# Optimization experiments

Measured on AMD Instinct MI355X. Metric: run time of the kernel, lower is better.

The kernel has to match this reference:

```python
import jax, jax.numpy as jnp
import numpy as np

C = 128  # num_hidden[-1]; nheads = 1 so dim == C
L, H, W = 16, 96, 96


def conv5(x, w):
    # x: [N, Cin, H, W], w: [1, Cin, 5, 5]; padding=2 -> SAME
    return jax.lax.conv_general_dilated(
        x, w, window_strides=(1, 1), padding=[(2, 2), (2, 2)],
        dimension_numbers=('NCHW', 'OIHW', 'NCHW'))


def setup_inputs() -> dict:
    key = jax.random.key(0)
    ks = jax.random.split(key, 9)
    s = 0.05
    return dict(
        x=jax.random.normal(ks[0], (L, C, H, W), jnp.float32),
        Wq=jax.random.normal(ks[1], (C, C), jnp.float32) * s,
        bq=jax.random.normal(ks[2], (C,), jnp.float32) * s,
        Wk=jax.random.normal(ks[3], (C, C), jnp.float32) * s,
        bk=jax.random.normal(ks[4], (C,), jnp.float32) * s,
        Wv=jax.random.normal(ks[5], (C, C), jnp.float32) * s,
        bv=jax.random.normal(ks[6], (C,), jnp.float32) * s,
        Wa=jax.random.normal(ks[7], (1, 2 * C, 5, 5), jnp.float32) * s,
        ba=jax.random.normal(ks[8], (1,), jnp.float32) * s,
    )


def reference(x, Wq, bq, Wk, bk, Wv, bv, Wa, ba):
    # 1x1 convs == per-pixel linear maps
    Q = jnp.einsum('lchw,dc->ldhw', x, Wq) + bq[None, :, None, None]
    K = jnp.einsum('lchw,dc->ldhw', x, Wk) + bk[None, :, None, None]
    V = jnp.einsum('lchw,dc->ldhw', x, Wv) + bv[None, :, None, None]
    # conv5x5(cat(Qi, Kj)) = conv5x5(Qi; Wa_q) + conv5x5(Kj; Wa_k) + ba
    Aq = conv5(Q, Wa[:, :C])[:, 0]   # [L, H, W]
    Ak = conv5(K, Wa[:, C:])[:, 0]   # [L, H, W]
    S = Aq[:, None] + Ak[None, :] + ba[0]       # [L, L, H, W] score maps H_ij
    A = jax.nn.softmax(S, axis=1)               # softmax over key frame j
    out = jnp.einsum('ijhw,jchw->ichw', A, V)   # weighted sum of V over j
    return out
```

## Files before the change

kernel.cpp:

```cpp
#include <hip/hip_runtime.h>


#define HW    9216
#define HDIM  96
#define WDIM  96
#define CDIM  128
#define WP    28

__device__ __forceinline__ void fma4(float4& a, const float4& x, const float4& s) {
    a.x += x.x * s.x; a.y += x.y * s.y; a.z += x.z * s.z; a.w += x.w * s.w;
}
__device__ __forceinline__ void axpy4(float4& o, float w, const float4& v) {
    o.x += w * v.x; o.y += w * v.y; o.z += w * v.z; o.w += w * v.w;
}

__global__ void k_prep(const float* __restrict__ Wk, const float* __restrict__ Wa,
                       const float* __restrict__ Wv,
                       float* __restrict__ weffp, float* __restrict__ wvt) {
    const int b = blockIdx.x;
    if (b < 14) {
        int idx = b * 256 + threadIdx.x;
        if (idx < 128 * WP) {
            int cp = idx / WP, tap = idx % WP;
            float s = 0.f;
            if (tap < 25)
                for (int c = 0; c < 128; ++c)
                    s += Wk[c * 128 + cp] * Wa[(128 + c) * 25 + tap];
            weffp[idx] = s;
        }
    } else {
        int idx = (b - 14) * 256 + threadIdx.x;
        wvt[(idx & 127) * 128 + (idx >> 7)] = Wv[idx];
    }
}

__global__ __launch_bounds__(256) void k_z(const float* __restrict__ x,
                                           const float* __restrict__ weffp,
                                           float* __restrict__ z) {
    __shared__ float red[4][25][64];
    const int tid  = threadIdx.x;
    const int wav  = __builtin_amdgcn_readfirstlane(tid >> 6);
    const int lane = tid & 63;
    const int j    = blockIdx.y;
    const int px0  = blockIdx.x * 128;

    const float* wg = weffp + wav * 32 * WP;
    const float* xb = x + ((size_t)j * CDIM + wav * 32) * HW + px0 + lane;

    float accA[25], accB[25];
    #pragma unroll
    for (int t = 0; t < 25; ++t) { accA[t] = 0.f; accB[t] = 0.f; }

    #pragma unroll 4
    for (int c = 0; c < 32; ++c) {
        const float* xc = xb + (size_t)c * HW;
        float xa = xc[0];
        float xbv = xc[64];
        #pragma unroll
        for (int t = 0; t < 25; ++t) {
            float wv = wg[c * WP + t];
            accA[t] = fmaf(wv, xa, accA[t]);
            accB[t] = fmaf(wv, xbv, accB[t]);
        }
    }

    float* zb = z + (size_t)j * 25 * HW + px0;

    #pragma unroll
    for (int t = 0; t < 25; ++t) red[wav][t][lane] = accA[t];
    __syncthreads();
    #pragma unroll
    for (int it = 0; it < 7; ++it) {
        int idx = it * 256 + tid;
        if (idx < 1600) {
            int t = idx >> 6, p = idx & 63;
            zb[(size_t)t * HW + p] = (red[0][t][p] + red[1][t][p])
                                   + (red[2][t][p] + red[3][t][p]);
        }
    }
    __syncthreads();

    #pragma unroll
    for (int t = 0; t < 25; ++t) red[wav][t][lane] = accB[t];
    __syncthreads();
    #pragma unroll
    for (int it = 0; it < 7; ++it) {
        int idx = it * 256 + tid;
        if (idx < 1600) {
            int t = idx >> 6, p = idx & 63;
            zb[(size_t)t * HW + 64 + p] = (red[0][t][p] + red[1][t][p])
                                        + (red[2][t][p] + red[3][t][p]);
        }
    }
}

__global__ __launch_bounds__(256) void k_ak(const float* __restrict__ z,
                                            float* __restrict__ ak) {
    const int j  = blockIdx.y;
    const int px = (blockIdx.x * 256 + threadIdx.x) * 4;
    const int h  = px / WDIM, cb = px % WDIM;
    const bool cok0 = (cb > 0);
    const bool cok2 = (cb < WDIM - 4);
    const float4 zf = make_float4(0.f, 0.f, 0.f, 0.f);
    const float* zb = z + (size_t)j * 25 * HW + px;

    float s0 = 0.f, s1 = 0.f, s2 = 0.f, s3 = 0.f;
    #pragma unroll
    for (int kh = 0; kh < 5; ++kh) {
        const bool rok = (unsigned)(h + kh - 2) < (unsigned)HDIM;
        const float* rp = zb + (kh * 5) * HW + (kh - 2) * WDIM;
        #pragma unroll
        for (int kw = 0; kw < 5; ++kw) {
            const float* tp = rp + kw * HW;
            float4 qa = (rok && cok0) ? *(const float4*)(tp - 4) : zf;
            float4 qb = (rok        ) ? *(const float4*)(tp)     : zf;
            float4 qc = (rok && cok2) ? *(const float4*)(tp + 4) : zf;
            float win[12] = {qa.x, qa.y, qa.z, qa.w, qb.x, qb.y, qb.z, qb.w,
                             qc.x, qc.y, qc.z, qc.w};
            s0 += win[kw + 2];
            s1 += win[kw + 3];
            s2 += win[kw + 4];
            s3 += win[kw + 5];
        }
    }
    float4 o = make_float4(s0, s1, s2, s3);
    *(float4*)(ak + (size_t)j * HW + px) = o;
}

__global__ __launch_bounds__(192) void k_conv(const float* __restrict__ x,
                                              const float* __restrict__ weffp,
                                              float* __restrict__ part) {
    const int j  = blockIdx.x;
    const int rt = blockIdx.y;
    const int g  = blockIdx.z;
    const int c0 = g * 16;
    __shared__ float tile[36 * 104];
    __shared__ float wsm[16 * WP];
    const int tid = threadIdx.x;
    for (int i = tid; i < 16 * WP; i += 192) wsm[i] = weffp[c0 * WP + i];
    const int cq = tid % 24;
    const int rg = tid / 24;
    const int r0 = rg * 4;
    const int rowbase = rt * 32;

    float4 acc[4];
    acc[0] = acc[1] = acc[2] = acc[3] = make_float4(0.f, 0.f, 0.f, 0.f);

    for (int ch = 0; ch < 16; ++ch) {
        const float* xc = x + (size_t)(j * CDIM + c0 + ch) * HW;
        __syncthreads();
        for (int idx = tid; idx < 36 * 26; idx += 192) {
            int r = idx / 26, q = idx % 26;
            int gr = rowbase - 2 + r;
            int gc = q * 4 - 4;
            float4 v = make_float4(0.f, 0.f, 0.f, 0.f);
            if (gr >= 0 && gr < HDIM && gc >= 0 && gc < WDIM)
                v = *(const float4*)(xc + gr * WDIM + gc);
            *(float4*)(tile + r * 104 + q * 4) = v;
        }
        __syncthreads();
        const float* wc = wsm + ch * WP;
        for (int rr = 0; rr < 8; ++rr) {
            const float* trow = tile + (r0 + rr) * 104 + cq * 4;
            float4 a  = *(const float4*)(trow);
            float4 b  = *(const float4*)(trow + 4);
            float4 c4 = *(const float4*)(trow + 8);
            float win[12] = {a.x, a.y, a.z, a.w, b.x, b.y, b.z, b.w,
                             c4.x, c4.y, c4.z, c4.w};
            #pragma unroll
            for (int orow = 0; orow < 4; ++orow) {
                int kh = rr - orow;
                if (kh < 0 || kh > 4) continue;
                #pragma unroll
                for (int kw = 0; kw < 5; ++kw) {
                    float w = wc[kh * 5 + kw];
                    acc[orow].x += w * win[kw + 2];
                    acc[orow].y += w * win[kw + 3];
                    acc[orow].z += w * win[kw + 4];
                    acc[orow].w += w * win[kw + 5];
                }
            }
        }
    }
    float* pr = part + (size_t)(g * 16 + j) * HW;
    #pragma unroll
    for (int orow = 0; orow < 4; ++orow) {
        int row = rowbase + r0 + orow;
        *(float4*)(pr + row * WDIM + cq * 4) = acc[orow];
    }
}

__global__ void k_combine(const float* __restrict__ part, float* __restrict__ ak) {
    const int j  = blockIdx.y;
    const int px = blockIdx.x * 256 + threadIdx.x;
    float s = 0.f;
    #pragma unroll
    for (int g = 0; g < 8; ++g) s += part[(size_t)(g * 16 + j) * HW + px];
    ak[(size_t)j * HW + px] = s;
}

__global__ __launch_bounds__(256) void k_xbar(const float* __restrict__ x,
                                              const float* __restrict__ ak,
                                              float* __restrict__ xbar) {
    const int b  = blockIdx.x;
    const int cp = b / 9;
    const int px = (b % 9) * 1024 + threadIdx.x * 4;

    float4 av[16];
    #pragma unroll
    for (int j = 0; j < 16; ++j)
        av[j] = *(const float4*)(ak + (size_t)j * HW + px);

    float4 m = av[0];
    #pragma unroll
    for (int j = 1; j < 16; ++j) {
        m.x = fmaxf(m.x, av[j].x); m.y = fmaxf(m.y, av[j].y);
        m.z = fmaxf(m.z, av[j].z); m.w = fmaxf(m.w, av[j].w);
    }
    float4 tot = make_float4(0.f, 0.f, 0.f, 0.f);
    #pragma unroll
    for (int j = 0; j < 16; ++j) {
        av[j].x = __expf(av[j].x - m.x); av[j].y = __expf(av[j].y - m.y);
        av[j].z = __expf(av[j].z - m.z); av[j].w = __expf(av[j].w - m.w);
        tot.x += av[j].x; tot.y += av[j].y; tot.z += av[j].z; tot.w += av[j].w;
    }
    float4 inv = make_float4(1.f / tot.x, 1.f / tot.y, 1.f / tot.z, 1.f / tot.w);

    float4 acc = make_float4(0.f, 0.f, 0.f, 0.f);
    #pragma unroll
    for (int j = 0; j < 16; ++j) {
        float4 xv = *(const float4*)(x + (size_t)(j * CDIM + cp) * HW + px);
        fma4(acc, xv, av[j]);
    }
    acc.x *= inv.x; acc.y *= inv.y; acc.z *= inv.z; acc.w *= inv.w;
    *(float4*)(xbar + (size_t)cp * HW + px) = acc;
}

__global__ __launch_bounds__(256) void k_mat(const float* __restrict__ xbar,
                                             const float* __restrict__ wvt,
                                             const float* __restrict__ bv,
                                             float* __restrict__ out) {
    __shared__ float lx[128 * 16];
    const int b    = blockIdx.x;
    const int half = blockIdx.y;
    const int tile = (b & 7) * 72 + (b >> 3);
    const int px0  = tile * 16;
    const int tid  = threadIdx.x;

    #pragma unroll
    for (int i = 0; i < 2; ++i) {
        int lin = tid + i * 256;
        int cp = lin >> 2, q = lin & 3;
        *(float4*)(lx + cp * 16 + q * 4) =
            *(const float4*)(xbar + (size_t)cp * HW + px0 + q * 4);
    }
    __syncthreads();

    const int q = tid & 3;
    const int c = half * 64 + (tid >> 2);
    float4 o = make_float4(0.f, 0.f, 0.f, 0.f);
    #pragma unroll 4
    for (int cp = 0; cp < 128; ++cp) {
        float4 xv = *(const float4*)(lx + cp * 16 + q * 4);
        axpy4(o, wvt[cp * 128 + c], xv);
    }
    float bb = bv[c];
    o.x += bb; o.y += bb; o.z += bb; o.w += bb;

    for (int i = 0; i < 16; ++i) {
        float* ob = out + (size_t)(i * CDIM + c) * HW + px0 + q * 4;
        *(float4*)(ob) = o;
    }
}

extern "C" void kernel_launch(void* const* d_in, const int* in_sizes, int n_in,
                              void* d_out, int out_size, void* d_ws, size_t ws_size,
                              hipStream_t stream) {
    const float* x  = (const float*)d_in[0];
    const float* Wk = (const float*)d_in[3];
    const float* Wv = (const float*)d_in[5];
    const float* bv = (const float*)d_in[6];
    const float* Wa = (const float*)d_in[7];
    float* out = (float*)d_out;

    char* ws = (char*)d_ws;
    float* weffp = (float*)(ws);
    float* wvt   = (float*)(ws + 16384);

    k_prep<<<78, 256, 0, stream>>>(Wk, Wa, Wv, weffp, wvt);

    const size_t Z_BYTES  = (size_t)16 * 25 * HW * 4;
    const size_t AK_BYTES = (size_t)16 * HW * 4;
    const size_t NEED_BIG = 81920 + Z_BYTES + AK_BYTES;

    if (ws_size >= NEED_BIG) {
        float* z   = (float*)(ws + 81920);
        float* akb = (float*)(ws + 81920 + Z_BYTES);
        float* xb  = (float*)(ws + 81920);
        k_z   <<<dim3(72, 16),  256, 0, stream>>>(x, weffp, z);
        k_ak  <<<dim3(9, 16),   256, 0, stream>>>(z, akb);
        k_xbar<<<1152,          256, 0, stream>>>(x, akb, xb);
        k_mat <<<dim3(576, 2),  256, 0, stream>>>(xb, wvt, bv, out);
    } else {
        float* part = (float*)(ws + 81920);
        float* akb  = (float*)(ws + 81920 + 4718592);
        float* xb   = (float*)(ws + 81920);
        k_conv   <<<dim3(16, 3, 8), 192, 0, stream>>>(x, weffp, part);
        k_combine<<<dim3(36, 16),   256, 0, stream>>>(part, akb);
        k_xbar   <<<1152,           256, 0, stream>>>(x, akb, xb);
        k_mat    <<<dim3(576, 2),   256, 0, stream>>>(xb, wvt, bv, out);
    }
}
```

Measured before the change: 74.06 us.

## Compute per-tap key projection z with bf16 MFMA instead of FP32 FMAs

Replaces the scalar FP32 k_z kernel, which accumulated 25 tap projections per pixel across four waves and reduced them through shared memory, with k_zm. The new kernel uses 16x16x32 bf16 MFMA instructions, with the effective weights pre-converted to bf16 by a new k_wb kernel and x converted to bf16 on the fly. This removes the LDS reduction and the large scalar FMA count, but lowers the precision of the attention logits and adds an extra small kernel launch. The x loads per lane are strided across channels, which may be less coalesced than before.

```diff
diff --git a/kernel.cpp b/kernel.cpp
--- a/kernel.cpp
+++ b/kernel.cpp
@@ -7,11 +7,20 @@
 #define CDIM  128
 #define WP    28
 
+typedef short s16x8  __attribute__((ext_vector_type(8)));
+typedef __bf16 bf16x8 __attribute__((ext_vector_type(8)));
+typedef float f32x4  __attribute__((ext_vector_type(4)));
+
 __device__ __forceinline__ void fma4(float4& a, const float4& x, const float4& s) {
     a.x += x.x * s.x; a.y += x.y * s.y; a.z += x.z * s.z; a.w += x.w * s.w;
 }
 __device__ __forceinline__ void axpy4(float4& o, float w, const float4& v) {
     o.x += w * v.x; o.y += w * v.y; o.z += w * v.z; o.w += w * v.w;
+}
+__device__ __forceinline__ short f2bf(float f) {
+    unsigned u = __float_as_uint(f);
+    unsigned r = u + 0x7FFFu + ((u >> 16) & 1u);
+    return (short)(r >> 16);
 }
 
 __global__ void k_prep(const float* __restrict__ Wk, const float* __restrict__ Wa,
@@ -34,62 +43,58 @@
     }
 }
 
-__global__ __launch_bounds__(256) void k_z(const float* __restrict__ x,
-                                           const float* __restrict__ weffp,
-                                           float* __restrict__ z) {
-    __shared__ float red[4][25][64];
+__global__ void k_wb(const float* __restrict__ weffp, short* __restrict__ weffb) {
+    int idx = blockIdx.x * 256 + threadIdx.x;
+    if (idx < 32 * 128) {
+        int t = idx >> 7, c = idx & 127;
+        float v = (t < 25) ? weffp[c * WP + t] : 0.f;
+        weffb[idx] = f2bf(v);
+    }
+}
+
+__global__ __launch_bounds__(256) void k_zm(const float* __restrict__ x,
+                                            const short* __restrict__ weffb,
+                                            float* __restrict__ z) {
     const int tid  = threadIdx.x;
-    const int wav  = __builtin_amdgcn_readfirstlane(tid >> 6);
+    const int wav  = tid >> 6;
     const int lane = tid & 63;
+    const int col  = lane & 15;
+    const int g    = lane >> 4;
     const int j    = blockIdx.y;
-    const int px0  = blockIdx.x * 128;
-
-    const float* wg = weffp + wav * 32 * WP;
-    const float* xb = x + ((size_t)j * CDIM + wav * 32) * HW + px0 + lane;
-
-    float accA[25], accB[25];
-    #pragma unroll
-    for (int t = 0; t < 25; ++t) { accA[t] = 0.f; accB[t] = 0.f; }
-
-    #pragma unroll 4
-    for (int c = 0; c < 32; ++c) {
-        const float* xc = xb + (size_t)c * HW;
-        float xa = xc[0];
-        float xbv = xc[64];
+    const int pxw  = blockIdx.x * 128 + wav * 32;
+
+    bf16x8 a[2][4];
+    #pragma unroll
+    for (int m = 0; m < 2; ++m)
         #pragma unroll
-        for (int t = 0; t < 25; ++t) {
-            float wv = wg[c * WP + t];
-            accA[t] = fmaf(wv, xa, accA[t]);
-            accB[t] = fmaf(wv, xbv, accB[t]);
-        }
-    }
-
-    float* zb = z + (size_t)j * 25 * HW + px0;
-
-    #pragma unroll
-    for (int t = 0; t < 25; ++t) red[wav][t][lane] = accA[t];
-    __syncthreads();
-    #pragma unroll
-    for (int it = 0; it < 7; ++it) {
-        int idx = it * 256 + tid;
-        if (idx < 1600) {
-            int t = idx >> 6, p = idx & 63;
-            zb[(size_t)t * HW + p] = (red[0][t][p] + red[1][t][p])
-                                   + (red[2][t][p] + red[3][t][p]);
-        }
-    }
-    __syncthreads();
-
-    #pragma unroll
-    for (int t = 0; t < 25; ++t) red[wav][t][lane] = accB[t];
-    __syncthreads();
-    #pragma unroll
-    for (int it = 0; it < 7; ++it) {
-        int idx = it * 256 + tid;
-        if (idx < 1600) {
-            int t = idx >> 6, p = idx & 63;
-            zb[(size_t)t * HW + 64 + p] = (red[0][t][p] + red[1][t][p])
-                                        + (red[2][t][p] + red[3][t][p]);
+        for (int ks = 0; ks < 4; ++ks)
+            a[m][ks] = __builtin_bit_cast(bf16x8,
+                *(const s16x8*)(weffb + (16 * m + col) * 128 + 32 * ks + 8 * g));
+
+    const float* xj = x + (size_t)j * CDIM * HW;
+    float* zj = z + (size_t)j * 25 * HW;
+
+    #pragma unroll
+    for (int nt = 0; nt < 2; ++nt) {
+        const int px = pxw + 16 * nt + col;
+        f32x4 acc0 = {0.f, 0.f, 0.f, 0.f};
+        f32x4 acc1 = {0.f, 0.f, 0.f, 0.f};
+        #pragma unroll
+        for (int ks = 0; ks < 4; ++ks) {
+            const float* xp = xj + (size_t)(32 * ks + 8 * g) * HW + px;
+            s16x8 s;
+            #pragma unroll
+            for (int i = 0; i < 8; ++i) s[i] = f2bf(xp[(size_t)i * HW]);
+            bf16x8 b = __builtin_bit_cast(bf16x8, s);
+            acc0 = __builtin_amdgcn_mfma_f32_16x16x32_bf16(a[0][ks], b, acc0, 0, 0, 0);
+            acc1 = __builtin_amdgcn_mfma_f32_16x16x32_bf16(a[1][ks], b, acc1, 0, 0, 0);
+        }
+        #pragma unroll
+        for (int r = 0; r < 4; ++r) {
+            zj[(size_t)(4 * g + r) * HW + px] = acc0[r];
+            int tap = 16 + 4 * g + r;
+            if (tap < 25)
+                zj[(size_t)tap * HW + px] = acc1[r];
         }
     }
 }
@@ -286,25 +291,27 @@
     char* ws = (char*)d_ws;
     float* weffp = (float*)(ws);
     float* wvt   = (float*)(ws + 16384);
+    short* weffb = (short*)(ws + 81920);
 
     k_prep<<<78, 256, 0, stream>>>(Wk, Wa, Wv, weffp, wvt);
 
     const size_t Z_BYTES  = (size_t)16 * 25 * HW * 4;
     const size_t AK_BYTES = (size_t)16 * HW * 4;
-    const size_t NEED_BIG = 81920 + Z_BYTES + AK_BYTES;
+    const size_t NEED_BIG = 90112 + Z_BYTES + AK_BYTES;
 
     if (ws_size >= NEED_BIG) {
-        float* z   = (float*)(ws + 81920);
-        float* akb = (float*)(ws + 81920 + Z_BYTES);
-        float* xb  = (float*)(ws + 81920);
-        k_z   <<<dim3(72, 16),  256, 0, stream>>>(x, weffp, z);
+        float* z   = (float*)(ws + 90112);
+        float* akb = (float*)(ws + 90112 + Z_BYTES);
+        float* xb  = (float*)(ws + 90112);
+        k_wb  <<<16,            256, 0, stream>>>(weffp, weffb);
+        k_zm  <<<dim3(72, 16),  256, 0, stream>>>(x, weffb, z);
         k_ak  <<<dim3(9, 16),   256, 0, stream>>>(z, akb);
         k_xbar<<<1152,          256, 0, stream>>>(x, akb, xb);
         k_mat <<<dim3(576, 2),  256, 0, stream>>>(xb, wvt, bv, out);
     } else {
-        float* part = (float*)(ws + 81920);
-        float* akb  = (float*)(ws + 81920 + 4718592);
-        float* xb   = (float*)(ws + 81920);
+        float* part = (float*)(ws + 90112);
+        float* akb  = (float*)(ws + 90112 + 4718592);
+        float* xb   = (float*)(ws + 90112);
         k_conv   <<<dim3(16, 3, 8), 192, 0, stream>>>(x, weffp, part);
         k_combine<<<dim3(36, 16),   256, 0, stream>>>(part, akb);
         k_xbar   <<<1152,           256, 0, stream>>>(x, akb, xb);
```

Measured after the change: 83.47 us. +12.7%, slower.
